# Optimization experiments

Hardware: AMD Instinct MI355X
Metric: run time of the kernel (lower is better)

Reference implementation:

```python
import jax, jax.numpy as jnp
import numpy as np
from jax import lax

DN = ('NCHW', 'OIHW', 'NCHW')


def conv2d(x, w, b, pad):
    y = lax.conv_general_dilated(x, w, (1, 1), [(pad, pad), (pad, pad)], dimension_numbers=DN)
    return y + b[None, :, None, None]


def unfold3x3(x):
    # x: [B, C, H, W] -> [B, C, 9, H, W], matching F.unfold(kernel=3, padding=1)
    B, C, H, W = x.shape
    xp = jnp.pad(x, ((0, 0), (0, 0), (1, 1), (1, 1)))
    views = [xp[:, :, ki:ki + H, kj:kj + W] for ki in range(3) for kj in range(3)]
    return jnp.stack(views, axis=2)


def setup_inputs() -> dict:
    key = jax.random.key(0)
    ks = jax.random.split(key, 4)
    B, C, H, W = 16, 1, 512, 512
    hid, up_h, up_w = 32, 1, 3
    x = jax.random.normal(ks[0], (B, C, H, W), dtype=jnp.float32)
    w1 = jax.random.normal(ks[1], (hid, C, 3, 3), dtype=jnp.float32) * (1.0 / 3.0)
    b1 = jnp.zeros((hid,), dtype=jnp.float32)
    alpha = jnp.full((hid,), 0.25, dtype=jnp.float32)  # PReLU init
    w2 = jax.random.normal(ks[2], (9 * up_h * up_w, hid, 1, 1), dtype=jnp.float32) * (1.0 / np.sqrt(hid))
    b2 = jnp.zeros((9 * up_h * up_w,), dtype=jnp.float32)
    return {"x": x, "target_h": H * up_h, "target_w": W * up_w,
            "w1": w1, "b1": b1, "alpha": alpha, "w2": w2, "b2": b2}


def reference(x, target_h, target_w, w1, b1, alpha, w2, b2):
    B, C, H, W = x.shape
    up_h = target_h // H  # = 1
    up_w = target_w // W  # = 3
    # mask_net: conv3x3 -> PReLU -> conv1x1
    h = conv2d(x, w1, b1, pad=1)
    h = jnp.where(h > 0, h, alpha[None, :, None, None] * h)
    mask = conv2d(h, w2, b2, pad=0)  # [B, 9*up_h*up_w, H, W]
    # convex upsample (anisotropic)
    neigh = unfold3x3(x)  # [B, C, 9, H, W]
    m = mask.reshape(B, 9, up_h, up_w, H, W)
    m = jax.nn.softmax(m, axis=1)
    up = jnp.einsum('bckhw,bkuvhw->bcuvhw', neigh, m)  # [B,C,up_h,up_w,H,W]
    up = up.transpose(0, 1, 4, 2, 5, 3)  # [B,C,H,up_h,W,up_w]
    return up.reshape(B, C, H * up_h, W * up_w)
```

## Files before the change

kernel.cpp:

```cpp
#include <hip/hip_runtime.h>
#include <hip/hip_bf16.h>


#define BB 16
#define HH 512
#define WW 512
#define HID 32
#define NM 27
#define LOG2E 1.44269504088896340736f
#define NT 16384
#define NBLK 1024

typedef short bf16x8 __attribute__((ext_vector_type(8)));
typedef float f32x4  __attribute__((ext_vector_type(4)));
typedef unsigned int u32;
typedef u32 u32x4 __attribute__((ext_vector_type(4)));
typedef u32 u32x2 __attribute__((ext_vector_type(2)));

__device__ __forceinline__ u32 pk2(float a, float b) {
    union { __hip_bfloat162 h2; u32 u; } cv;
    cv.h2 = __float22bfloat162_rn(make_float2(a, b));
    return cv.u;
}

__device__ __forceinline__ void lds_fence() {
    asm volatile("" ::: "memory");
    __builtin_amdgcn_sched_barrier(0);
}

__device__ __forceinline__ void load_xv(const float* __restrict__ x, int tile,
                                        int tid, float xv[9]) {
    const int p    = tile * 256 + tid;
    const int wcol = p & (WW - 1);
    const int t    = p >> 9;
    const int hrow = t & (HH - 1);
    const int bidx = t >> 9;
    const float* xb = x + (size_t)bidx * (HH * WW);
#pragma unroll
    for (int ki = 0; ki < 3; ++ki) {
        const int hy = hrow + ki - 1;
        const bool hok = (unsigned)hy < (unsigned)HH;
#pragma unroll
        for (int kj = 0; kj < 3; ++kj) {
            const int wx = wcol + kj - 1;
            const bool ok = hok && ((unsigned)wx < (unsigned)WW);
            xv[ki * 3 + kj] = ok ? xb[hy * WW + wx] : 0.0f;
        }
    }
}

__global__ void prep_B(const float* __restrict__ w1, const float* __restrict__ b1,
                       const float* __restrict__ alpha, const float* __restrict__ w2,
                       const float* __restrict__ b2, __hip_bfloat16* __restrict__ ws) {
    const int i = blockIdx.x * 256 + threadIdx.x;
    if (i >= 6144) return;
    float v = 0.0f;
    int tm;
    if (i < 4096) {
        tm = i >> 11;
        const int r = i & 2047, n = r >> 6, k = r & 63;
        if (n < NM) {
            if (k < 9) {
                for (int c = 0; c < HID; ++c)
                    v += w2[n * HID + c] * (0.5f * (1.0f + alpha[c])) * w1[c * 9 + k];
            } else if (k == 9) {
                v = b2[n];
                for (int c = 0; c < HID; ++c)
                    v += w2[n * HID + c] * (0.5f * (1.0f + alpha[c])) * b1[c];
            } else if (k >= 32) {
                const int c = k - 32;
                v = w2[n * HID + c] * (0.5f * (1.0f - alpha[c]));
            }
        }
        v *= LOG2E;
    } else {
        const int j = i - 4096;
        tm = j >> 10;
        const int r = j & 1023, n = r >> 5, k = r & 31;
        v = (k < 9) ? w1[n * 9 + k] : (k == 9 ? b1[n] : 0.0f);
    }
    const float hi = __bfloat162float(__float2bfloat16(v));
    ws[i] = __float2bfloat16(tm == 0 ? v : v - hi);
}

__global__ __launch_bounds__(256, 4) void convex_upsample_mfma5(
    const float* __restrict__ x,
    const __hip_bfloat16* __restrict__ ws,
    float* __restrict__ out)
{
    __shared__ char lds_raw[4][64 * 128];

    const int tid  = threadIdx.x;
    const int wv   = tid >> 6;
    const int lane = tid & 63;
    const int l16  = lane & 15;
    const int lq   = lane >> 4;
    char* wbase = lds_raw[wv];
    const int sx  = (lane & 7) << 4;
    const int asx = (l16 & 7) << 4;

    bf16x8 Bf2[2][2][2];
    bf16x8 Bf1[2][2];
#pragma unroll
    for (int tm = 0; tm < 2; ++tm)
#pragma unroll
        for (int nt = 0; nt < 2; ++nt) {
#pragma unroll
            for (int kt = 0; kt < 2; ++kt)
                Bf2[tm][kt][nt] = *(const bf16x8*)(ws + tm * 2048 + (nt * 16 + l16) * 64 + kt * 32 + lq * 8);
            Bf1[tm][nt] = *(const bf16x8*)(ws + 4096 + tm * 1024 + (nt * 16 + l16) * 32 + lq * 8);
        }

    int tb = blockIdx.x;
    float xv[9];
    load_xv(x, tb, tid, xv);

    while (tb < NT) {
        const int tn  = tb + NBLK;
        const int tpf = (tn < NT) ? tn : 0;
        float xn[9];
        load_xv(x, tpf, tid, xn);

        char* myrow = wbase + lane * 128;
        *(u32x4*)(myrow + (0 ^ sx))  = (u32x4){pk2(xv[0], xv[1]), pk2(xv[2], xv[3]),
                                               pk2(xv[4], xv[5]), pk2(xv[6], xv[7])};
        *(u32x4*)(myrow + (16 ^ sx)) = (u32x4){pk2(xv[8], 1.0f), 0u, 0u, 0u};
        *(u32x4*)(myrow + (32 ^ sx)) = (u32x4){0u, 0u, 0u, 0u};
        *(u32x4*)(myrow + (48 ^ sx)) = (u32x4){0u, 0u, 0u, 0u};

        lds_fence();

        bf16x8 a0[4];
#pragma unroll
        for (int mt = 0; mt < 4; ++mt) {
            char* ab = wbase + (mt * 16 + l16) * 128;
            a0[mt] = *(const bf16x8*)(ab + ((lq * 16) ^ asx));
            f32x4 z0 = {0.f, 0.f, 0.f, 0.f}, z1 = {0.f, 0.f, 0.f, 0.f};
            z0 = __builtin_amdgcn_mfma_f32_16x16x32_bf16(Bf1[0][0], a0[mt], z0, 0, 0, 0);
            z0 = __builtin_amdgcn_mfma_f32_16x16x32_bf16(Bf1[1][0], a0[mt], z0, 0, 0, 0);
            z1 = __builtin_amdgcn_mfma_f32_16x16x32_bf16(Bf1[0][1], a0[mt], z1, 0, 0, 0);
            z1 = __builtin_amdgcn_mfma_f32_16x16x32_bf16(Bf1[1][1], a0[mt], z1, 0, 0, 0);
            const u32x2 d0 = (u32x2){pk2(fabsf(z0[0]), fabsf(z0[1])), pk2(fabsf(z0[2]), fabsf(z0[3]))};
            const u32x2 d1 = (u32x2){pk2(fabsf(z1[0]), fabsf(z1[1])), pk2(fabsf(z1[2]), fabsf(z1[3]))};
            const int nb0 = 64 + lq * 8;
            const int nb1 = 96 + lq * 8;
            *(u32x2*)(ab + ((nb0 & 0x70) ^ asx) + (nb0 & 15)) = d0;
            *(u32x2*)(ab + ((nb1 & 0x70) ^ asx) + (nb1 & 15)) = d1;
        }

        lds_fence();

#pragma unroll
        for (int mt = 0; mt < 4; ++mt) {
            char* ab = wbase + (mt * 16 + l16) * 128;
            const bf16x8 a1 = *(const bf16x8*)(ab + ((64 + lq * 16) ^ asx));
            f32x4 c0 = {0.f, 0.f, 0.f, 0.f}, c1 = {0.f, 0.f, 0.f, 0.f};
            c0 = __builtin_amdgcn_mfma_f32_16x16x32_bf16(Bf2[0][0][0], a0[mt], c0, 0, 0, 0);
            c0 = __builtin_amdgcn_mfma_f32_16x16x32_bf16(Bf2[0][1][0], a1,     c0, 0, 0, 0);
            c0 = __builtin_amdgcn_mfma_f32_16x16x32_bf16(Bf2[1][0][0], a0[mt], c0, 0, 0, 0);
            c0 = __builtin_amdgcn_mfma_f32_16x16x32_bf16(Bf2[1][1][0], a1,     c0, 0, 0, 0);
            c1 = __builtin_amdgcn_mfma_f32_16x16x32_bf16(Bf2[0][0][1], a0[mt], c1, 0, 0, 0);
            c1 = __builtin_amdgcn_mfma_f32_16x16x32_bf16(Bf2[0][1][1], a1,     c1, 0, 0, 0);
            c1 = __builtin_amdgcn_mfma_f32_16x16x32_bf16(Bf2[1][0][1], a0[mt], c1, 0, 0, 0);
            c1 = __builtin_amdgcn_mfma_f32_16x16x32_bf16(Bf2[1][1][1], a1,     c1, 0, 0, 0);
            *(f32x4*)(ab + ((lq * 16) ^ asx))      = c0;
            *(f32x4*)(ab + ((64 + lq * 16) ^ asx)) = c1;
        }

        lds_fence();

        f32x4 mv[7];
#pragma unroll
        for (int q = 0; q < 7; ++q)
            mv[q] = *(const f32x4*)(myrow + ((q * 16) ^ sx));

        const int p    = tb * 256 + tid;
        const int wcol = p & (WW - 1);
        const int t    = p >> 9;
        const int hrow = t & (HH - 1);
        const int bidx = t >> 9;
        const size_t ob = ((size_t)(bidx * HH + hrow) * (WW * 3)) + (size_t)wcol * 3;
#pragma unroll
        for (int v = 0; v < 3; ++v) {
            float ssum = 0.0f, acc = 0.0f;
#pragma unroll
            for (int k = 0; k < 9; ++k) {
                const int j = k * 3 + v;
                const float e = __builtin_amdgcn_exp2f(mv[j >> 2][j & 3]);
                ssum += e;
                acc = fmaf(xv[k], e, acc);
            }
            out[ob + v] = acc * __builtin_amdgcn_rcpf(ssum);
        }

        lds_fence();

        tb = tn;
#pragma unroll
        for (int k = 0; k < 9; ++k) xv[k] = xn[k];
    }
}

extern "C" void kernel_launch(void* const* d_in, const int* in_sizes, int n_in,
                              void* d_out, int out_size, void* d_ws, size_t ws_size,
                              hipStream_t stream) {
    const float* x     = (const float*)d_in[0];
    const float* w1    = (const float*)d_in[3];
    const float* b1    = (const float*)d_in[4];
    const float* alpha = (const float*)d_in[5];
    const float* w2    = (const float*)d_in[6];
    const float* b2    = (const float*)d_in[7];
    float* out = (float*)d_out;
    __hip_bfloat16* ws = (__hip_bfloat16*)d_ws;

    hipLaunchKernelGGL(prep_B, dim3(24), dim3(256), 0, stream, w1, b1, alpha, w2, b2, ws);
    hipLaunchKernelGGL(convex_upsample_mfma5, dim3(NBLK), dim3(256), 0, stream,
                       x, ws, out);
}
```

Measured before the change: 70.13 us.

## Drop bf16 hi/lo split MFMAs, double grid, and use clamped unconditional neighbor loads

Removes the second (residual) bf16 term of the weight split so each GEMM stage issues half as many MFMA instructions. It also doubles the persistent grid size and rewrites the 3x3 neighbor gather to use clamped addresses with a select instead of predicated loads. Dropping the low-order weight correction reduces the effective precision of the mask logits, which may exceed tolerance.

```diff
diff --git a/kernel.cpp b/kernel.cpp
--- a/kernel.cpp
+++ b/kernel.cpp
@@ -9,7 +9,7 @@
 #define NM 27
 #define LOG2E 1.44269504088896340736f
 #define NT 16384
-#define NBLK 1024
+#define NBLK 2048
 
 typedef short bf16x8 __attribute__((ext_vector_type(8)));
 typedef float f32x4  __attribute__((ext_vector_type(4)));
@@ -36,17 +36,24 @@
     const int hrow = t & (HH - 1);
     const int bidx = t >> 9;
     const float* xb = x + (size_t)bidx * (HH * WW);
-#pragma unroll
-    for (int ki = 0; ki < 3; ++ki) {
-        const int hy = hrow + ki - 1;
-        const bool hok = (unsigned)hy < (unsigned)HH;
+    int hy[3], wx[3];
+    bool hok[3], wok[3];
+#pragma unroll
+    for (int i = 0; i < 3; ++i) {
+        const int h = hrow + i - 1;
+        hok[i] = (unsigned)h < (unsigned)HH;
+        hy[i]  = h < 0 ? 0 : (h > HH - 1 ? HH - 1 : h);
+        const int w = wcol + i - 1;
+        wok[i] = (unsigned)w < (unsigned)WW;
+        wx[i]  = w < 0 ? 0 : (w > WW - 1 ? WW - 1 : w);
+    }
+#pragma unroll
+    for (int ki = 0; ki < 3; ++ki)
 #pragma unroll
         for (int kj = 0; kj < 3; ++kj) {
-            const int wx = wcol + kj - 1;
-            const bool ok = hok && ((unsigned)wx < (unsigned)WW);
-            xv[ki * 3 + kj] = ok ? xb[hy * WW + wx] : 0.0f;
-        }
-    }
+            const float v = xb[hy[ki] * WW + wx[kj]];
+            xv[ki * 3 + kj] = (hok[ki] && wok[kj]) ? v : 0.0f;
+        }
 }
 
 __global__ void prep_B(const float* __restrict__ w1, const float* __restrict__ b1,
@@ -83,7 +90,7 @@
     ws[i] = __float2bfloat16(tm == 0 ? v : v - hi);
 }
 
-__global__ __launch_bounds__(256, 4) void convex_upsample_mfma5(
+__global__ __launch_bounds__(256, 4) void convex_upsample_mfma6(
     const float* __restrict__ x,
     const __hip_bfloat16* __restrict__ ws,
     float* __restrict__ out)
@@ -99,17 +106,15 @@
     const int sx  = (lane & 7) << 4;
     const int asx = (l16 & 7) << 4;
 
-    bf16x8 Bf2[2][2][2];
-    bf16x8 Bf1[2][2];
-#pragma unroll
-    for (int tm = 0; tm < 2; ++tm)
-#pragma unroll
-        for (int nt = 0; nt < 2; ++nt) {
-#pragma unroll
-            for (int kt = 0; kt < 2; ++kt)
-                Bf2[tm][kt][nt] = *(const bf16x8*)(ws + tm * 2048 + (nt * 16 + l16) * 64 + kt * 32 + lq * 8);
-            Bf1[tm][nt] = *(const bf16x8*)(ws + 4096 + tm * 1024 + (nt * 16 + l16) * 32 + lq * 8);
-        }
+    bf16x8 Bf2[2][2];
+    bf16x8 Bf1[2];
+#pragma unroll
+    for (int nt = 0; nt < 2; ++nt) {
+#pragma unroll
+        for (int kt = 0; kt < 2; ++kt)
+            Bf2[kt][nt] = *(const bf16x8*)(ws + (nt * 16 + l16) * 64 + kt * 32 + lq * 8);
+        Bf1[nt] = *(const bf16x8*)(ws + 4096 + (nt * 16 + l16) * 32 + lq * 8);
+    }
 
     int tb = blockIdx.x;
     float xv[9];
@@ -136,10 +141,8 @@
             char* ab = wbase + (mt * 16 + l16) * 128;
             a0[mt] = *(const bf16x8*)(ab + ((lq * 16) ^ asx));
             f32x4 z0 = {0.f, 0.f, 0.f, 0.f}, z1 = {0.f, 0.f, 0.f, 0.f};
-            z0 = __builtin_amdgcn_mfma_f32_16x16x32_bf16(Bf1[0][0], a0[mt], z0, 0, 0, 0);
-            z0 = __builtin_amdgcn_mfma_f32_16x16x32_bf16(Bf1[1][0], a0[mt], z0, 0, 0, 0);
-            z1 = __builtin_amdgcn_mfma_f32_16x16x32_bf16(Bf1[0][1], a0[mt], z1, 0, 0, 0);
-            z1 = __builtin_amdgcn_mfma_f32_16x16x32_bf16(Bf1[1][1], a0[mt], z1, 0, 0, 0);
+            z0 = __builtin_amdgcn_mfma_f32_16x16x32_bf16(Bf1[0], a0[mt], z0, 0, 0, 0);
+            z1 = __builtin_amdgcn_mfma_f32_16x16x32_bf16(Bf1[1], a0[mt], z1, 0, 0, 0);
             const u32x2 d0 = (u32x2){pk2(fabsf(z0[0]), fabsf(z0[1])), pk2(fabsf(z0[2]), fabsf(z0[3]))};
             const u32x2 d1 = (u32x2){pk2(fabsf(z1[0]), fabsf(z1[1])), pk2(fabsf(z1[2]), fabsf(z1[3]))};
             const int nb0 = 64 + lq * 8;
@@ -155,14 +158,10 @@
             char* ab = wbase + (mt * 16 + l16) * 128;
             const bf16x8 a1 = *(const bf16x8*)(ab + ((64 + lq * 16) ^ asx));
             f32x4 c0 = {0.f, 0.f, 0.f, 0.f}, c1 = {0.f, 0.f, 0.f, 0.f};
-            c0 = __builtin_amdgcn_mfma_f32_16x16x32_bf16(Bf2[0][0][0], a0[mt], c0, 0, 0, 0);
-            c0 = __builtin_amdgcn_mfma_f32_16x16x32_bf16(Bf2[0][1][0], a1,     c0, 0, 0, 0);
-            c0 = __builtin_amdgcn_mfma_f32_16x16x32_bf16(Bf2[1][0][0], a0[mt], c0, 0, 0, 0);
-            c0 = __builtin_amdgcn_mfma_f32_16x16x32_bf16(Bf2[1][1][0], a1,     c0, 0, 0, 0);
-            c1 = __builtin_amdgcn_mfma_f32_16x16x32_bf16(Bf2[0][0][1], a0[mt], c1, 0, 0, 0);
-            c1 = __builtin_amdgcn_mfma_f32_16x16x32_bf16(Bf2[0][1][1], a1,     c1, 0, 0, 0);
-            c1 = __builtin_amdgcn_mfma_f32_16x16x32_bf16(Bf2[1][0][1], a0[mt], c1, 0, 0, 0);
-            c1 = __builtin_amdgcn_mfma_f32_16x16x32_bf16(Bf2[1][1][1], a1,     c1, 0, 0, 0);
+            c0 = __builtin_amdgcn_mfma_f32_16x16x32_bf16(Bf2[0][0], a0[mt], c0, 0, 0, 0);
+            c0 = __builtin_amdgcn_mfma_f32_16x16x32_bf16(Bf2[1][0], a1,     c0, 0, 0, 0);
+            c1 = __builtin_amdgcn_mfma_f32_16x16x32_bf16(Bf2[0][1], a0[mt], c1, 0, 0, 0);
+            c1 = __builtin_amdgcn_mfma_f32_16x16x32_bf16(Bf2[1][1], a1,     c1, 0, 0, 0);
             *(f32x4*)(ab + ((lq * 16) ^ asx))      = c0;
             *(f32x4*)(ab + ((64 + lq * 16) ^ asx)) = c1;
         }
@@ -214,6 +213,6 @@
     __hip_bfloat16* ws = (__hip_bfloat16*)d_ws;
 
     hipLaunchKernelGGL(prep_B, dim3(24), dim3(256), 0, stream, w1, b1, alpha, w2, b2, ws);
-    hipLaunchKernelGGL(convex_upsample_mfma5, dim3(NBLK), dim3(256), 0, stream,
+    hipLaunchKernelGGL(convex_upsample_mfma6, dim3(NBLK), dim3(256), 0, stream,
                        x, ws, out);
 }
```

New measurement: 72.64 us. 3.6% more time.
